# Optimization experiments

Measured on AMD Instinct MI355X. Metric: run time of the kernel, lower is better.

Reference implementation:

```python
import jax, jax.numpy as jnp
import numpy as np
from functools import partial

# Module hyperparameters (from init_kwargs)
T, C_IN, H, W_DIM = 128, 16, 64, 64
C_OUT, KH, KW = 64, 3, 3
PAD = ((1, 1), (1, 1))  # (top,bottom),(left,right) -> symmetric here
STRIDES = (1, 1)
F_V_THRESH = 8.0
F_V_THRESH_LOW = -1.0
F_V_RESET = 0.0
# fVSubtract is None -> reset-to-value branch


def setup_inputs() -> dict:
    key = jax.random.key(0)
    kx, kw, kb = jax.random.split(key, 3)
    x = jax.random.uniform(kx, (T, C_IN, H, W_DIM), dtype=jnp.float32)
    fan_in = C_IN * KH * KW
    bound = 1.0 / np.sqrt(fan_in)
    W = jax.random.uniform(kw, (C_OUT, C_IN, KH, KW), dtype=jnp.float32,
                           minval=-bound, maxval=bound)
    b = jax.random.uniform(kb, (C_OUT,), dtype=jnp.float32,
                           minval=-bound, maxval=bound)
    return {"x": x, "W": W, "b": b}


def _spiking_conv(x, W, b):
    # conv over all timesteps at once (time is the conv batch dim): [T, C_out, H, W]
    conv_out = jax.lax.conv_general_dilated(
        x, W, window_strides=STRIDES, padding=PAD,
        dimension_numbers=("NCHW", "OIHW", "NCHW"))
    conv_out = conv_out + b[None, :, None, None]

    def step(state, conv_t):
        state = state + conv_t
        spikes = (state >= F_V_THRESH).astype(conv_t.dtype)
        # reset-to-value branch (fVSubtract is None)
        state = spikes * F_V_RESET + state * (1.0 - spikes)
        # nn.Threshold(v, v): x if x > v else v
        state = jnp.where(state > F_V_THRESH_LOW, state, F_V_THRESH_LOW)
        return state, spikes

    init_state = jnp.zeros(conv_out.shape[1:], dtype=conv_out.dtype)
    _, num_spikes = jax.lax.scan(step, init_state, conv_out)
    return num_spikes  # [T, C_out, H, W] float (0/1)


def reference(x, W, b):
    return _spiking_conv(x, W, b)
```

## Files before the change

kernel.cpp:

```cpp
#include <hip/hip_runtime.h>

#define T_STEPS 128
#define CIN     16
#define HH      64
#define WW      64
#define COUT    64
#define HWSZ    (HH * WW)
#define CHW     (COUT * HWSZ)
#define XCHW    (CIN * HWSZ)

#define TILE    32
#define HALO    34
#define LSTR    36
#define PLANE   (HALO * LSTR)
#define NST     (CIN * HALO * HALO)
#define WBLK    40

__global__ void transpose_w(const float* __restrict__ W, float* __restrict__ Wtr) {
    int e = blockIdx.x * 256 + threadIdx.x;
    if (e >= COUT * CIN * 9) return;
    int co = e / (CIN * 9);
    int r  = e - co * (CIN * 9);
    int ci = r / 9;
    int k  = r - ci * 9;
    Wtr[((co >> 2) * CIN + ci) * WBLK + (co & 3) * 9 + k] = W[e];
}

__global__ __launch_bounds__(512, 4)
void spiking_conv_pass1(const float* __restrict__ x, const float* __restrict__ Wtr,
                        const float* __restrict__ b, float* __restrict__ out) {
    __shared__ float xs[CIN * PLANE];

    const int tid = threadIdx.x;
    const int t   = blockIdx.y;
    const int h0  = (blockIdx.x >> 1) * TILE;
    const int w0  = (blockIdx.x & 1) * TILE;
    const int coh = blockIdx.z;

    const float* xt = x + t * XCHW;
    {
        float vbuf[19]; int ibuf[19];
#pragma unroll
        for (int k = 0; k < 18; ++k) {
            unsigned e = tid + k * 512;
            unsigned ci = e / (HALO * HALO);
            unsigned rem = e - ci * (HALO * HALO);
            unsigned r  = rem / HALO;
            unsigned c  = rem - r * HALO;
            int gh = h0 - 1 + (int)r;
            int gw = w0 - 1 + (int)c;
            bool inb = (unsigned)gh < HH && (unsigned)gw < WW;
            vbuf[k] = inb ? xt[ci * HWSZ + gh * WW + gw] : 0.f;
            ibuf[k] = ci * PLANE + r * LSTR + c;
        }
#pragma unroll
        for (int k = 0; k < 18; ++k) xs[ibuf[k]] = vbuf[k];
#pragma unroll
        for (int k = 0; k < 19; ++k) {
            unsigned e = tid + (18 + k) * 512;
            unsigned ci = e / (HALO * HALO);
            unsigned rem = e - ci * (HALO * HALO);
            unsigned r  = rem / HALO;
            unsigned c  = rem - r * HALO;
            int gh = h0 - 1 + (int)r;
            int gw = w0 - 1 + (int)c;
            bool inb = e < NST && (unsigned)gh < HH && (unsigned)gw < WW;
            vbuf[k] = inb ? xt[ci * HWSZ + gh * WW + gw] : 0.f;
            ibuf[k] = (e < NST) ? (int)(ci * PLANE + r * LSTR + c) : -1;
        }
#pragma unroll
        for (int k = 0; k < 19; ++k)
            if (ibuf[k] >= 0) xs[ibuf[k]] = vbuf[k];
    }
    __syncthreads();

    const int cog = __builtin_amdgcn_readfirstlane(tid >> 8);
    const int sp  = tid & 255;
    const int pr0 = sp >> 3;
    const int pc0 = (sp & 7) * 4;
    float* outt = out + t * CHW;

    float acc[16][4];
#pragma unroll
    for (int j = 0; j < 16; ++j)
#pragma unroll
        for (int p = 0; p < 4; ++p) acc[j][p] = 0.f;

#pragma unroll 1
    for (int ci = 0; ci < CIN; ++ci) {
        float xv[3][6];
#pragma unroll
        for (int dr = 0; dr < 3; ++dr) {
            const float* row = &xs[ci * PLANE + (pr0 + dr) * LSTR + pc0];
            float4 a  = *(const float4*)row;
            float2 c2 = *(const float2*)(row + 4);
            xv[dr][0] = a.x;  xv[dr][1] = a.y;
            xv[dr][2] = a.z;  xv[dr][3] = a.w;
            xv[dr][4] = c2.x; xv[dr][5] = c2.y;
        }
#pragma unroll
        for (int g = 0; g < 4; ++g) {
            const int g4 = coh * 8 + cog * 4 + g;
            const float* wb = Wtr + (g4 * CIN + ci) * WBLK;
            float w[36];
#pragma unroll
            for (int i = 0; i < 36; ++i) w[i] = wb[i];
#pragma unroll
            for (int jj = 0; jj < 4; ++jj)
#pragma unroll
                for (int ky = 0; ky < 3; ++ky)
#pragma unroll
                    for (int kx = 0; kx < 3; ++kx) {
                        const float wv = w[jj * 9 + ky * 3 + kx];
#pragma unroll
                        for (int p = 0; p < 4; ++p)
                            acc[g * 4 + jj][p] += wv * xv[ky][kx + p];
                    }
        }
    }

#pragma unroll
    for (int g = 0; g < 4; ++g)
#pragma unroll
        for (int jj = 0; jj < 4; ++jj) {
            const int co = coh * 32 + cog * 16 + g * 4 + jj;
            const float bias = b[co];
            float4 o;
            o.x = acc[g * 4 + jj][0] + bias;
            o.y = acc[g * 4 + jj][1] + bias;
            o.z = acc[g * 4 + jj][2] + bias;
            o.w = acc[g * 4 + jj][3] + bias;
            *(float4*)&outt[co * HWSZ + (h0 + pr0) * WW + (w0 + pc0)] = o;
        }
}

__global__ __launch_bounds__(256)
void spiking_scan_pass2(float* __restrict__ io) {
    const int idx = blockIdx.x * 256 + threadIdx.x;
    float* p = io + idx;
    float s = 0.f;
    float v[8], nv[8];
#pragma unroll
    for (int i = 0; i < 8; ++i) v[i] = p[(size_t)i * CHW];
#pragma unroll 1
    for (int tb = 0; tb < 15; ++tb) {
#pragma unroll
        for (int i = 0; i < 8; ++i) nv[i] = p[(size_t)((tb + 1) * 8 + i) * CHW];
#pragma unroll
        for (int i = 0; i < 8; ++i) {
            s += v[i];
            bool a = (s >= 8.0f);
            float o = a ? 1.f : 0.f;
            s = a ? 0.f : s;
            s = fmaxf(s, -1.f);
            p[(size_t)(tb * 8 + i) * CHW] = o;
        }
#pragma unroll
        for (int i = 0; i < 8; ++i) v[i] = nv[i];
    }
#pragma unroll
    for (int i = 0; i < 8; ++i) {
        s += v[i];
        bool a = (s >= 8.0f);
        float o = a ? 1.f : 0.f;
        s = a ? 0.f : s;
        s = fmaxf(s, -1.f);
        p[(size_t)(120 + i) * CHW] = o;
    }
}

extern "C" void kernel_launch(void* const* d_in, const int* in_sizes, int n_in,
                              void* d_out, int out_size, void* d_ws, size_t ws_size,
                              hipStream_t stream) {
    const float* x = (const float*)d_in[0];
    const float* W = (const float*)d_in[1];
    const float* b = (const float*)d_in[2];
    float* out = (float*)d_out;
    float* Wtr = (float*)d_ws;

    transpose_w<<<36, 256, 0, stream>>>(W, Wtr);

    dim3 g1(4, 128, 2);
    spiking_conv_pass1<<<g1, 512, 0, stream>>>(x, Wtr, b, out);

    spiking_scan_pass2<<<CHW / 256, 256, 0, stream>>>(out);
}
```

Measured before the change: 269.4 us.

## Read conv inputs directly from global memory, reorder weights, deepen scan prefetch

The conv kernel no longer stages the haloed input tile in shared memory. Each thread now reads its rows straight from global memory, using clamped edge loads and masking, and the barrier is gone. Weights are re-laid out by kernel row so each row's weights for four output channels load as three float4s. The scan pass now double-buffers two groups of eight timesteps to keep more loads in flight and uses nontemporal stores for the spike output. The cost is redundant global/L1 traffic for overlapping halo reads, in exchange for dropping the LDS fill and sync.

```diff
diff --git a/kernel.cpp b/kernel.cpp
--- a/kernel.cpp
+++ b/kernel.cpp
@@ -10,11 +10,6 @@
 #define XCHW    (CIN * HWSZ)
 
 #define TILE    32
-#define HALO    34
-#define LSTR    36
-#define PLANE   (HALO * LSTR)
-#define NST     (CIN * HALO * HALO)
-#define WBLK    40
 
 __global__ void transpose_w(const float* __restrict__ W, float* __restrict__ Wtr) {
     int e = blockIdx.x * 256 + threadIdx.x;
@@ -23,61 +18,26 @@
     int r  = e - co * (CIN * 9);
     int ci = r / 9;
     int k  = r - ci * 9;
-    Wtr[((co >> 2) * CIN + ci) * WBLK + (co & 3) * 9 + k] = W[e];
+    int ky = k / 3;
+    int kx = k - ky * 3;
+    Wtr[((co >> 2) * CIN + ci) * 36 + ky * 12 + (co & 3) * 3 + kx] = W[e];
 }
 
 __global__ __launch_bounds__(512, 4)
 void spiking_conv_pass1(const float* __restrict__ x, const float* __restrict__ Wtr,
                         const float* __restrict__ b, float* __restrict__ out) {
-    __shared__ float xs[CIN * PLANE];
-
     const int tid = threadIdx.x;
     const int t   = blockIdx.y;
     const int h0  = (blockIdx.x >> 1) * TILE;
     const int w0  = (blockIdx.x & 1) * TILE;
     const int coh = blockIdx.z;
 
-    const float* xt = x + t * XCHW;
-    {
-        float vbuf[19]; int ibuf[19];
-#pragma unroll
-        for (int k = 0; k < 18; ++k) {
-            unsigned e = tid + k * 512;
-            unsigned ci = e / (HALO * HALO);
-            unsigned rem = e - ci * (HALO * HALO);
-            unsigned r  = rem / HALO;
-            unsigned c  = rem - r * HALO;
-            int gh = h0 - 1 + (int)r;
-            int gw = w0 - 1 + (int)c;
-            bool inb = (unsigned)gh < HH && (unsigned)gw < WW;
-            vbuf[k] = inb ? xt[ci * HWSZ + gh * WW + gw] : 0.f;
-            ibuf[k] = ci * PLANE + r * LSTR + c;
-        }
-#pragma unroll
-        for (int k = 0; k < 18; ++k) xs[ibuf[k]] = vbuf[k];
-#pragma unroll
-        for (int k = 0; k < 19; ++k) {
-            unsigned e = tid + (18 + k) * 512;
-            unsigned ci = e / (HALO * HALO);
-            unsigned rem = e - ci * (HALO * HALO);
-            unsigned r  = rem / HALO;
-            unsigned c  = rem - r * HALO;
-            int gh = h0 - 1 + (int)r;
-            int gw = w0 - 1 + (int)c;
-            bool inb = e < NST && (unsigned)gh < HH && (unsigned)gw < WW;
-            vbuf[k] = inb ? xt[ci * HWSZ + gh * WW + gw] : 0.f;
-            ibuf[k] = (e < NST) ? (int)(ci * PLANE + r * LSTR + c) : -1;
-        }
-#pragma unroll
-        for (int k = 0; k < 19; ++k)
-            if (ibuf[k] >= 0) xs[ibuf[k]] = vbuf[k];
-    }
-    __syncthreads();
-
     const int cog = __builtin_amdgcn_readfirstlane(tid >> 8);
     const int sp  = tid & 255;
     const int pr0 = sp >> 3;
     const int pc0 = (sp & 7) * 4;
+
+    const float* xt = x + t * XCHW;
     float* outt = out + t * CHW;
 
     float acc[16][4];
@@ -86,36 +46,53 @@
 #pragma unroll
         for (int p = 0; p < 4; ++p) acc[j][p] = 0.f;
 
+    const int gw0 = w0 + pc0;
+    const bool colL = (gw0 > 0);
+    const bool colR = (gw0 + 4 < WW);
+    const int gwl = colL ? gw0 - 1 : 0;
+    const int gwr = colR ? gw0 + 4 : WW - 1;
+
 #pragma unroll 1
     for (int ci = 0; ci < CIN; ++ci) {
         float xv[3][6];
 #pragma unroll
         for (int dr = 0; dr < 3; ++dr) {
-            const float* row = &xs[ci * PLANE + (pr0 + dr) * LSTR + pc0];
-            float4 a  = *(const float4*)row;
-            float2 c2 = *(const float2*)(row + 4);
-            xv[dr][0] = a.x;  xv[dr][1] = a.y;
-            xv[dr][2] = a.z;  xv[dr][3] = a.w;
-            xv[dr][4] = c2.x; xv[dr][5] = c2.y;
+            const int gh = h0 + pr0 + dr - 1;
+            const bool rowOK = (unsigned)gh < (unsigned)HH;
+            const int ghc = rowOK ? gh : 0;
+            const float* rp = xt + ci * HWSZ + ghc * WW;
+            float4 m  = *(const float4*)(rp + gw0);
+            float  xl = rp[gwl];
+            float  xr = rp[gwr];
+            xv[dr][0] = (rowOK && colL) ? xl : 0.f;
+            xv[dr][1] = rowOK ? m.x : 0.f;
+            xv[dr][2] = rowOK ? m.y : 0.f;
+            xv[dr][3] = rowOK ? m.z : 0.f;
+            xv[dr][4] = rowOK ? m.w : 0.f;
+            xv[dr][5] = (rowOK && colR) ? xr : 0.f;
         }
 #pragma unroll
-        for (int g = 0; g < 4; ++g) {
-            const int g4 = coh * 8 + cog * 4 + g;
-            const float* wb = Wtr + (g4 * CIN + ci) * WBLK;
-            float w[36];
+        for (int dr = 0; dr < 3; ++dr) {
 #pragma unroll
-            for (int i = 0; i < 36; ++i) w[i] = wb[i];
+            for (int g = 0; g < 4; ++g) {
+                const int g4 = coh * 8 + cog * 4 + g;
+                const float* wr = Wtr + (g4 * CIN + ci) * 36 + dr * 12;
+                float4 wA = *(const float4*)(wr);
+                float4 wB = *(const float4*)(wr + 4);
+                float4 wC = *(const float4*)(wr + 8);
+                const float wf[12] = {wA.x, wA.y, wA.z, wA.w,
+                                      wB.x, wB.y, wB.z, wB.w,
+                                      wC.x, wC.y, wC.z, wC.w};
 #pragma unroll
-            for (int jj = 0; jj < 4; ++jj)
-#pragma unroll
-                for (int ky = 0; ky < 3; ++ky)
+                for (int jj = 0; jj < 4; ++jj)
 #pragma unroll
                     for (int kx = 0; kx < 3; ++kx) {
-                        const float wv = w[jj * 9 + ky * 3 + kx];
+                        const float wv = wf[jj * 3 + kx];
 #pragma unroll
                         for (int p = 0; p < 4; ++p)
-                            acc[g * 4 + jj][p] += wv * xv[ky][kx + p];
+                            acc[g * 4 + jj][p] += wv * xv[dr][kx + p];
                     }
+            }
         }
     }
 
@@ -139,33 +116,57 @@
     const int idx = blockIdx.x * 256 + threadIdx.x;
     float* p = io + idx;
     float s = 0.f;
-    float v[8], nv[8];
+    float A[8], B[8];
 #pragma unroll
-    for (int i = 0; i < 8; ++i) v[i] = p[(size_t)i * CHW];
+    for (int i = 0; i < 8; ++i) A[i] = p[(size_t)i * CHW];
+#pragma unroll
+    for (int i = 0; i < 8; ++i) B[i] = p[(size_t)(8 + i) * CHW];
 #pragma unroll 1
-    for (int tb = 0; tb < 15; ++tb) {
-#pragma unroll
-        for (int i = 0; i < 8; ++i) nv[i] = p[(size_t)((tb + 1) * 8 + i) * CHW];
+    for (int tb = 0; tb < 7; ++tb) {
+        const size_t base = (size_t)tb * 16 * CHW;
 #pragma unroll
         for (int i = 0; i < 8; ++i) {
-            s += v[i];
+            s += A[i];
             bool a = (s >= 8.0f);
             float o = a ? 1.f : 0.f;
             s = a ? 0.f : s;
             s = fmaxf(s, -1.f);
-            p[(size_t)(tb * 8 + i) * CHW] = o;
+            __builtin_nontemporal_store(o, &p[base + (size_t)i * CHW]);
         }
 #pragma unroll
-        for (int i = 0; i < 8; ++i) v[i] = nv[i];
+        for (int i = 0; i < 8; ++i) A[i] = p[base + (size_t)(16 + i) * CHW];
+#pragma unroll
+        for (int i = 0; i < 8; ++i) {
+            s += B[i];
+            bool a = (s >= 8.0f);
+            float o = a ? 1.f : 0.f;
+            s = a ? 0.f : s;
+            s = fmaxf(s, -1.f);
+            __builtin_nontemporal_store(o, &p[base + (size_t)(8 + i) * CHW]);
+        }
+#pragma unroll
+        for (int i = 0; i < 8; ++i) B[i] = p[base + (size_t)(24 + i) * CHW];
     }
+    {
+        const size_t base = (size_t)112 * CHW;
 #pragma unroll
-    for (int i = 0; i < 8; ++i) {
-        s += v[i];
-        bool a = (s >= 8.0f);
-        float o = a ? 1.f : 0.f;
-        s = a ? 0.f : s;
-        s = fmaxf(s, -1.f);
-        p[(size_t)(120 + i) * CHW] = o;
+        for (int i = 0; i < 8; ++i) {
+            s += A[i];
+            bool a = (s >= 8.0f);
+            float o = a ? 1.f : 0.f;
+            s = a ? 0.f : s;
+            s = fmaxf(s, -1.f);
+            __builtin_nontemporal_store(o, &p[base + (size_t)i * CHW]);
+        }
+#pragma unroll
+        for (int i = 0; i < 8; ++i) {
+            s += B[i];
+            bool a = (s >= 8.0f);
+            float o = a ? 1.f : 0.f;
+            s = a ? 0.f : s;
+            s = fmaxf(s, -1.f);
+            __builtin_nontemporal_store(o, &p[base + (size_t)(8 + i) * CHW]);
+        }
     }
 }
 
```

Result: slower. 288.4 us (+7.1%).
